# Performance work log

Measured on AMD Instinct MI355X. Metric: run time of the kernel, lower is better.

The kernel has to match this reference:

```python
import jax, jax.numpy as jnp
import numpy as np

M_MARGIN = 0.25
GAMMA = 256.0
NEG_INF = jnp.float32(-1e30)


def setup_inputs() -> dict:
    key = jax.random.key(0)
    k1, k2 = jax.random.split(key)
    feature = jax.random.normal(k1, (8192, 128), dtype=jnp.float32)
    label = jax.random.randint(k2, (8192,), 0, 64, dtype=jnp.int64)
    return {"feature": feature, "label": label}


def reference(feature, label):
    # F.normalize: L2-normalize rows (eps=1e-12)
    norm = jnp.maximum(jnp.linalg.norm(feature, axis=1, keepdims=True), 1e-12)
    f = feature / norm
    sim = f @ f.T  # [N, N]
    N = sim.shape[0]

    same = label[:, None] == label[None, :]
    triu = jnp.triu(jnp.ones((N, N), dtype=bool), k=1)
    pos_mask = same & triu
    neg_mask = (~same) & triu

    sim_d = jax.lax.stop_gradient(sim)  # .detach() in original
    ap = jnp.maximum(-sim_d + 1.0 + M_MARGIN, 0.0)
    an = jnp.maximum(sim_d + M_MARGIN, 0.0)
    delta_p = 1.0 - M_MARGIN
    delta_n = M_MARGIN

    logit_p = -ap * (sim - delta_p) * GAMMA
    logit_n = an * (sim - delta_n) * GAMMA

    # boolean-gather + logsumexp == masked logsumexp (fixed shapes, jit-friendly)
    lse_p = jax.nn.logsumexp(jnp.where(pos_mask, logit_p, NEG_INF))
    lse_n = jax.nn.logsumexp(jnp.where(neg_mask, logit_n, NEG_INF))

    return jax.nn.softplus(lse_n + lse_p)
```

## Files before the change

kernel.cpp:

```cpp
#include <hip/hip_runtime.h>
#include <hip/hip_bf16.h>
#include <math.h>

#define NROW 8192
#define DIM  128
#define BM   64
#define BN   128
#define NBLK   2080
#define NTILES (NBLK * 2)
#define NT4    (NTILES * 4)
#define NRED   32
#define PERRED (NT4 / NRED)

typedef __bf16 bf16x8 __attribute__((ext_vector_type(8)));
typedef float  f32x4  __attribute__((ext_vector_type(4)));

#define G2     369.3299304675746f
#define QPOS   (0.9375f * G2)
#define QNEG   (-0.0625f * G2)
#define NEGBIG (-3.0e38f)
#define MSENT  (-4000.0f)
#define CSTR   32

__global__ __launch_bounds__(256)
void hist_kernel(const int* __restrict__ lab, int* __restrict__ cursor) {
    __shared__ int h[4][64];
    const int tid  = threadIdx.x;
    const int w    = tid >> 6;
    const int lane = tid & 63;
    h[w][lane] = 0;
    __syncthreads();
    for (int i = tid; i < NROW; i += 256)
        atomicAdd(&h[w][lab[i]], 1);
    __syncthreads();
    if (tid < 64) {
        int tot = h[0][tid] + h[1][tid] + h[2][tid] + h[3][tid];
        int v = tot;
        #pragma unroll
        for (int off = 1; off < 64; off <<= 1) {
            int u = __shfl_up(v, off, 64);
            if (tid >= off) v += u;
        }
        cursor[tid * CSTR] = v - tot;
    }
}

__global__ __launch_bounds__(256)
void prep_kernel(const float* __restrict__ f, const int* __restrict__ lab,
                 int* __restrict__ cursor,
                 __hip_bfloat16* __restrict__ fhi, int* __restrict__ labS) {
    int row  = blockIdx.x * 4 + (threadIdx.x >> 6);
    int lane = threadIdx.x & 63;
    float2 v = ((const float2*)(f + (size_t)row * DIM))[lane];
    float ss = v.x * v.x + v.y * v.y;
    #pragma unroll
    for (int off = 32; off; off >>= 1) ss += __shfl_xor(ss, off, 64);
    float inv = 1.0f / fmaxf(sqrtf(ss), 1e-12f);
    int l = lab[row];
    int dest = 0;
    if (lane == 0) dest = atomicAdd(&cursor[l * CSTR], 1);
    dest = __shfl(dest, 0, 64);
    __hip_bfloat162 hv;
    hv.x = __float2bfloat16(v.x * inv);
    hv.y = __float2bfloat16(v.y * inv);
    ((__hip_bfloat162*)(fhi + (size_t)dest * DIM))[lane] = hv;
    if (lane == 0) labS[dest] = l;
}

__global__ __launch_bounds__(256, 2)
void sim_kernel(const __hip_bfloat16* __restrict__ fhi,
                const int* __restrict__ labS,
                float4* __restrict__ blockRes) {
    const int tid  = threadIdx.x;
    const int w    = tid >> 6;
    const int lane = tid & 63;
    const int lrow = lane & 15;
    const int lk   = lane >> 4;

    int bid = blockIdx.x;
    int tc = (int)((sqrtf(8.f * (float)bid + 1.f) - 1.f) * 0.5f);
    if (tc > 63) tc = 63;
    while (tc > 0 && bid < (tc * (tc + 1)) / 2) --tc;
    while (bid >= ((tc + 1) * (tc + 2)) / 2) ++tc;
    const int chunk = bid - (tc * (tc + 1)) / 2;
    const bool edge = (chunk == tc);

    const int colBase  = tc * BN;
    const int rowBase0 = (2 * chunk) * BM;
    const int rowBase1 = rowBase0 + BM;

    __shared__ __align__(16) char smem[64 * 1024];
    char* Bs = smem;
    char* A0 = smem + 32 * 1024;
    char* A1 = smem + 48 * 1024;

    const int rsub4 = lane >> 4;
    const int col16 = (lane & 15) << 4;

    #pragma unroll
    for (int t = 0; t < 8; ++t) {
        int seg  = w * 8 + t;
        int brow = seg * 4 + rsub4;
        const char* g = (const char*)fhi + (size_t)(colBase + brow) * 256
                      + (col16 ^ ((brow & 7) << 4));
        __builtin_amdgcn_global_load_lds(
            (const __attribute__((address_space(1))) void*)g,
            (__attribute__((address_space(3))) void*)(Bs + seg * 1024), 16, 0, 0);
    }
    #pragma unroll
    for (int t = 0; t < 4; ++t) {
        int seg  = w * 4 + t;
        int arow = seg * 4 + rsub4;
        int swz  = (col16 ^ ((arow & 7) << 4));
        const char* g0 = (const char*)fhi + (size_t)(rowBase0 + arow) * 256 + swz;
        const char* g1 = (const char*)fhi + (size_t)(rowBase1 + arow) * 256 + swz;
        __builtin_amdgcn_global_load_lds(
            (const __attribute__((address_space(1))) void*)g0,
            (__attribute__((address_space(3))) void*)(A0 + seg * 1024), 16, 0, 0);
        __builtin_amdgcn_global_load_lds(
            (const __attribute__((address_space(1))) void*)g1,
            (__attribute__((address_space(3))) void*)(A1 + seg * 1024), 16, 0, 0);
    }

    const int labCol0 = labS[colBase];
    const int labRE0  = labS[rowBase0 + BM - 1];
    const int labRE1  = labS[rowBase1 + BM - 1];

    const int ncol0 = w * 32;

    __syncthreads();

    f32x4 acc[4][2];

    #pragma unroll
    for (int ti = 0; ti < 2; ++ti) {
        const char* As      = ti ? A1 : A0;
        const int   rowBase = ti ? rowBase1 : rowBase0;
        const int   labRE   = ti ? labRE1 : labRE0;

        #pragma unroll
        for (int mi = 0; mi < 4; ++mi)
            #pragma unroll
            for (int ni = 0; ni < 2; ++ni) acc[mi][ni] = (f32x4){0.f, 0.f, 0.f, 0.f};

        #pragma unroll
        for (int q = 0; q < 4; ++q) {
            const int kb = q * 64 + lk * 16;
            bf16x8 bfr[2];
            #pragma unroll
            for (int ni = 0; ni < 2; ++ni) {
                int rb = ncol0 + ni * 16 + lrow;
                bfr[ni] = *(const bf16x8*)(Bs + rb * 256 + (kb ^ ((rb & 7) << 4)));
            }
            #pragma unroll
            for (int mi = 0; mi < 4; ++mi) {
                int ra = mi * 16 + lrow;
                bf16x8 afr = *(const bf16x8*)(As + ra * 256 + (kb ^ ((ra & 7) << 4)));
                #pragma unroll
                for (int ni = 0; ni < 2; ++ni)
                    acc[mi][ni] = __builtin_amdgcn_mfma_f32_16x16x32_bf16(
                        afr, bfr[ni], acc[mi][ni], 0, 0, 0);
            }
        }

        const bool mixed = edge || (labRE == labCol0);
        float4 res;
        if (!mixed) {
            float mx = 0.0f;
            #pragma unroll
            for (int mi = 0; mi < 4; ++mi)
                #pragma unroll
                for (int ni = 0; ni < 2; ++ni)
                    #pragma unroll
                    for (int r = 0; r < 4; ++r) {
                        float t = fmaxf(acc[mi][ni][r], -0.25f);
                        acc[mi][ni][r] = t;
                        mx = fmaxf(mx, fabsf(t));
                    }
            #pragma unroll
            for (int off = 32; off; off >>= 1)
                mx = fmaxf(mx, __shfl_xor(mx, off, 64));
            const float zc = -G2 * mx * mx;
            float sn = 0.f;
            #pragma unroll
            for (int mi = 0; mi < 4; ++mi)
                #pragma unroll
                for (int ni = 0; ni < 2; ++ni)
                    #pragma unroll
                    for (int r = 0; r < 4; ++r) {
                        float t = acc[mi][ni][r];
                        sn += __builtin_amdgcn_exp2f(fmaf(G2, t * t, zc));
                    }
            #pragma unroll
            for (int off = 32; off; off >>= 1)
                sn += __shfl_xor(sn, off, 64);
            res = make_float4(MSENT, 0.f, fmaf(G2, mx * mx, QNEG), sn);
        } else {
            int lbv[2];
            #pragma unroll
            for (int ni = 0; ni < 2; ++ni)
                lbv[ni] = labS[colBase + ncol0 + ni * 16 + lrow];
            int4 laR[4];
            #pragma unroll
            for (int mi = 0; mi < 4; ++mi)
                laR[mi] = *(const int4*)&labS[rowBase + mi * 16 + lk * 4];

            float minp = 1e30f;
            float mabs = -1.0f;

#define PASS_AB(EDGEF)                                                         \
    _Pragma("unroll")                                                          \
    for (int mi = 0; mi < 4; ++mi) {                                           \
        const int la[4] = {laR[mi].x, laR[mi].y, laR[mi].z, laR[mi].w};        \
        _Pragma("unroll")                                                      \
        for (int ni = 0; ni < 2; ++ni) {                                       \
            _Pragma("unroll")                                                  \
            for (int r = 0; r < 4; ++r) {                                      \
                float s = acc[mi][ni][r];                                      \
                bool pos = (la[r] == lbv[ni]);                                 \
                float t = fmaxf(s, -0.25f);                                    \
                bool valid = true;                                             \
                if (EDGEF) {                                                   \
                    int ig = rowBase + mi * 16 + lk * 4 + r;                   \
                    int jg = colBase + ncol0 + ni * 16 + lrow;                 \
                    valid = (jg > ig);                                         \
                    pos = pos && valid;                                        \
                }                                                              \
                float u = pos ? s : t;                                         \
                minp = fminf(minp, pos ? s : 1e30f);                           \
                bool nm = EDGEF ? (valid && !pos) : !pos;                      \
                mabs = fmaxf(mabs, nm ? fabsf(t) : -1.0f);                     \
                acc[mi][ni][r] = u;                                            \
            }                                                                  \
        }                                                                      \
    }
            if (edge) { PASS_AB(true) } else { PASS_AB(false) }
#undef PASS_AB

            #pragma unroll
            for (int off = 32; off; off >>= 1) {
                minp = fminf(minp, __shfl_xor(minp, off, 64));
                mabs = fmaxf(mabs, __shfl_xor(mabs, off, 64));
            }
            const float Mp = (minp < 2.0f)
                ? fmaf(G2, minp * minp, fmaf(-2.0f * G2, minp, QPOS)) : MSENT;
            const float Mn = (mabs >= 0.0f) ? fmaf(G2, mabs * mabs, QNEG) : MSENT;
            const float qph = QPOS - Mp;
            const float qnh = QNEG - Mn;
            float sp = 0.f, sn = 0.f;

#define PASS_B(EDGEF)                                                          \
    _Pragma("unroll")                                                          \
    for (int mi = 0; mi < 4; ++mi) {                                           \
        const int la[4] = {laR[mi].x, laR[mi].y, laR[mi].z, laR[mi].w};        \
        _Pragma("unroll")                                                      \
        for (int ni = 0; ni < 2; ++ni) {                                       \
            _Pragma("unroll")                                                  \
            for (int r = 0; r < 4; ++r) {                                      \
                float u = acc[mi][ni][r];                                      \
                bool pos = (la[r] == lbv[ni]);                                 \
                float P  = pos ? (-2.0f * G2) : 0.0f;                          \
                float Qh = pos ? qph : qnh;                                    \
                float e = __builtin_amdgcn_exp2f(                              \
                              fmaf(G2, u * u, fmaf(P, u, Qh)));                \
                if (EDGEF) {                                                   \
                    int ig = rowBase + mi * 16 + lk * 4 + r;                   \
                    int jg = colBase + ncol0 + ni * 16 + lrow;                 \
                    e = (jg > ig) ? e : 0.f;                                   \
                }                                                              \
                float ep = pos ? e : 0.f;                                      \
                sp += ep;                                                      \
                sn += (e - ep);                                                \
            }                                                                  \
        }                                                                      \
    }
            if (edge) { PASS_B(true) } else { PASS_B(false) }
#undef PASS_B

            #pragma unroll
            for (int off = 32; off; off >>= 1) {
                sp += __shfl_xor(sp, off, 64);
                sn += __shfl_xor(sn, off, 64);
            }
            res = make_float4(Mp, sp, Mn, sn);
        }
        if (lane == 0) blockRes[(bid * 2 + ti) * 4 + w] = res;
    }
}

__device__ __forceinline__ void merge2(float& m, float& s, float mo, float so) {
    float M = fmaxf(m, mo);
    s = s * __builtin_amdgcn_exp2f(m - M) + so * __builtin_amdgcn_exp2f(mo - M);
    m = M;
}

__global__ __launch_bounds__(256)
void reduce_kernel(const float4* __restrict__ in, float4* __restrict__ partial) {
    __shared__ float red[4][4];
    const int tid  = threadIdx.x;
    const int base = blockIdx.x * PERRED;
    float mp = NEGBIG, sp = 0.f, mn = NEGBIG, sn = 0.f;
    for (int i = tid; i < PERRED; i += 256) {
        float4 v = in[base + i];
        merge2(mp, sp, v.x, v.y);
        merge2(mn, sn, v.z, v.w);
    }
    #pragma unroll
    for (int off = 32; off; off >>= 1) {
        float mo = __shfl_xor(mp, off, 64), so = __shfl_xor(sp, off, 64);
        merge2(mp, sp, mo, so);
        float mo2 = __shfl_xor(mn, off, 64), so2 = __shfl_xor(sn, off, 64);
        merge2(mn, sn, mo2, so2);
    }
    const int wv = tid >> 6;
    if ((tid & 63) == 0) {
        red[wv][0] = mp; red[wv][1] = sp; red[wv][2] = mn; red[wv][3] = sn;
    }
    __syncthreads();
    if (tid == 0) {
        mp = red[0][0]; sp = red[0][1]; mn = red[0][2]; sn = red[0][3];
        #pragma unroll
        for (int q = 1; q < 4; ++q) {
            merge2(mp, sp, red[q][0], red[q][1]);
            merge2(mn, sn, red[q][2], red[q][3]);
        }
        partial[blockIdx.x] = make_float4(mp, sp, mn, sn);
    }
}

__global__ __launch_bounds__(64)
void finalize_kernel(const float4* __restrict__ partial, float* __restrict__ out) {
    const int lane = threadIdx.x;
    float mp = NEGBIG, sp = 0.f, mn = NEGBIG, sn = 0.f;
    if (lane < NRED) {
        float4 v = partial[lane];
        mp = v.x; sp = v.y; mn = v.z; sn = v.w;
    }
    #pragma unroll
    for (int off = 32; off; off >>= 1) {
        float mo = __shfl_xor(mp, off, 64), so = __shfl_xor(sp, off, 64);
        merge2(mp, sp, mo, so);
        float mo2 = __shfl_xor(mn, off, 64), so2 = __shfl_xor(sn, off, 64);
        merge2(mn, sn, mo2, so2);
    }
    if (lane == 0) {
        const double LN2 = 0.6931471805599453;
        double lse_p = ((double)mp + log2((double)sp)) * LN2;
        double lse_n = ((double)mn + log2((double)sn)) * LN2;
        double xx = lse_p + lse_n;
        double r = (xx > 30.0) ? xx : log1p(exp(xx));
        out[0] = (float)r;
    }
}

extern "C" void kernel_launch(void* const* d_in, const int* in_sizes, int n_in,
                              void* d_out, int out_size, void* d_ws, size_t ws_size,
                              hipStream_t stream) {
    const float* f   = (const float*)d_in[0];
    const int*   lab = (const int*)d_in[1];
    float*  out      = (float*)d_out;

    __hip_bfloat16* fhi = (__hip_bfloat16*)d_ws;
    int* labS    = (int*)((char*)d_ws + 2u * 1024 * 1024);
    int* cursor  = (int*)((char*)d_ws + 3u * 1024 * 1024);
    float4* blockRes = (float4*)((char*)d_ws + 4u * 1024 * 1024);
    float4* partial  = (float4*)((char*)d_ws + 8u * 1024 * 1024);

    hist_kernel<<<1, 256, 0, stream>>>(lab, cursor);
    prep_kernel<<<NROW / 4, 256, 0, stream>>>(f, lab, cursor, fhi, labS);
    sim_kernel<<<NBLK, 256, 0, stream>>>(fhi, labS, blockRes);
    reduce_kernel<<<NRED, 256, 0, stream>>>(blockRes, partial);
    finalize_kernel<<<1, 64, 0, stream>>>(partial, out);
}
```

Measured before the change: 46.74 us.

## Drop label sorting and use square 128x128 tiles with 512-thread blocks

Removes the histogram/counting-sort pass that grouped rows by label, so prep only normalizes rows in place. The similarity kernel now processes square 128x128 upper-triangular tiles with 8 waves per block and caches labels in LDS. The specialized pure-negative fast path that relied on sorted labels is gone, so every tile runs the two-pass masked logsumexp. This saves a kernel launch and atomics but adds more exp work per tile.

```diff
diff --git a/kernel.cpp b/kernel.cpp
--- a/kernel.cpp
+++ b/kernel.cpp
@@ -4,11 +4,10 @@
 
 #define NROW 8192
 #define DIM  128
-#define BM   64
-#define BN   128
-#define NBLK   2080
-#define NTILES (NBLK * 2)
-#define NT4    (NTILES * 4)
+#define BT   128
+#define NT   (NROW / BT)
+#define NBLK ((NT * (NT + 1)) / 2)
+#define NT4  (NBLK * 8)
 #define NRED   32
 #define PERRED (NT4 / NRED)
 
@@ -20,35 +19,9 @@
 #define QNEG   (-0.0625f * G2)
 #define NEGBIG (-3.0e38f)
 #define MSENT  (-4000.0f)
-#define CSTR   32
 
 __global__ __launch_bounds__(256)
-void hist_kernel(const int* __restrict__ lab, int* __restrict__ cursor) {
-    __shared__ int h[4][64];
-    const int tid  = threadIdx.x;
-    const int w    = tid >> 6;
-    const int lane = tid & 63;
-    h[w][lane] = 0;
-    __syncthreads();
-    for (int i = tid; i < NROW; i += 256)
-        atomicAdd(&h[w][lab[i]], 1);
-    __syncthreads();
-    if (tid < 64) {
-        int tot = h[0][tid] + h[1][tid] + h[2][tid] + h[3][tid];
-        int v = tot;
-        #pragma unroll
-        for (int off = 1; off < 64; off <<= 1) {
-            int u = __shfl_up(v, off, 64);
-            if (tid >= off) v += u;
-        }
-        cursor[tid * CSTR] = v - tot;
-    }
-}
-
-__global__ __launch_bounds__(256)
-void prep_kernel(const float* __restrict__ f, const int* __restrict__ lab,
-                 int* __restrict__ cursor,
-                 __hip_bfloat16* __restrict__ fhi, int* __restrict__ labS) {
+void prep_kernel(const float* __restrict__ f, __hip_bfloat16* __restrict__ fhi) {
     int row  = blockIdx.x * 4 + (threadIdx.x >> 6);
     int lane = threadIdx.x & 63;
     float2 v = ((const float2*)(f + (size_t)row * DIM))[lane];
@@ -56,20 +29,15 @@
     #pragma unroll
     for (int off = 32; off; off >>= 1) ss += __shfl_xor(ss, off, 64);
     float inv = 1.0f / fmaxf(sqrtf(ss), 1e-12f);
-    int l = lab[row];
-    int dest = 0;
-    if (lane == 0) dest = atomicAdd(&cursor[l * CSTR], 1);
-    dest = __shfl(dest, 0, 64);
     __hip_bfloat162 hv;
     hv.x = __float2bfloat16(v.x * inv);
     hv.y = __float2bfloat16(v.y * inv);
-    ((__hip_bfloat162*)(fhi + (size_t)dest * DIM))[lane] = hv;
-    if (lane == 0) labS[dest] = l;
-}
-
-__global__ __launch_bounds__(256, 2)
+    ((__hip_bfloat162*)(fhi + (size_t)row * DIM))[lane] = hv;
+}
+
+__global__ __launch_bounds__(512, 4)
 void sim_kernel(const __hip_bfloat16* __restrict__ fhi,
-                const int* __restrict__ labS,
+                const int* __restrict__ lab,
                 float4* __restrict__ blockRes) {
     const int tid  = threadIdx.x;
     const int w    = tid >> 6;
@@ -78,137 +46,85 @@
     const int lk   = lane >> 4;
 
     int bid = blockIdx.x;
-    int tc = (int)((sqrtf(8.f * (float)bid + 1.f) - 1.f) * 0.5f);
-    if (tc > 63) tc = 63;
-    while (tc > 0 && bid < (tc * (tc + 1)) / 2) --tc;
-    while (bid >= ((tc + 1) * (tc + 2)) / 2) ++tc;
-    const int chunk = bid - (tc * (tc + 1)) / 2;
-    const bool edge = (chunk == tc);
-
-    const int colBase  = tc * BN;
-    const int rowBase0 = (2 * chunk) * BM;
-    const int rowBase1 = rowBase0 + BM;
+    int tr = (int)((129.0f - sqrtf(16641.0f - 8.0f * (float)bid)) * 0.5f);
+    while (tr > 0 && bid < tr * NT - (tr * (tr - 1)) / 2) --tr;
+    while (bid >= (tr + 1) * NT - ((tr + 1) * tr) / 2) ++tr;
+    const int tc = tr + (bid - (tr * NT - (tr * (tr - 1)) / 2));
+
+    const int rowBase = tr * BT;
+    const int colBase = tc * BT;
+    const bool edge = (tr == tc);
 
     __shared__ __align__(16) char smem[64 * 1024];
-    char* Bs = smem;
-    char* A0 = smem + 32 * 1024;
-    char* A1 = smem + 48 * 1024;
+    __shared__ int labA[BT];
+    __shared__ int labB[BT];
+    char* As = smem;
+    char* Bs = smem + 32 * 1024;
+
+    if (tid < BT)            labA[tid] = lab[rowBase + tid];
+    else if (tid < 2 * BT)   labB[tid - BT] = lab[colBase + (tid - BT)];
 
     const int rsub4 = lane >> 4;
     const int col16 = (lane & 15) << 4;
 
     #pragma unroll
     for (int t = 0; t < 8; ++t) {
-        int seg  = w * 8 + t;
-        int brow = seg * 4 + rsub4;
-        const char* g = (const char*)fhi + (size_t)(colBase + brow) * 256
-                      + (col16 ^ ((brow & 7) << 4));
+        int seg = w * 8 + t;
+        int arr = seg >> 5;
+        int s32 = seg & 31;
+        int row = s32 * 4 + rsub4;
+        const char* g = (const char*)fhi
+            + (size_t)((arr ? colBase : rowBase) + row) * 256
+            + (col16 ^ ((row & 7) << 4));
+        char* ldsb = (arr ? Bs : As) + s32 * 1024;
         __builtin_amdgcn_global_load_lds(
             (const __attribute__((address_space(1))) void*)g,
-            (__attribute__((address_space(3))) void*)(Bs + seg * 1024), 16, 0, 0);
-    }
-    #pragma unroll
-    for (int t = 0; t < 4; ++t) {
-        int seg  = w * 4 + t;
-        int arow = seg * 4 + rsub4;
-        int swz  = (col16 ^ ((arow & 7) << 4));
-        const char* g0 = (const char*)fhi + (size_t)(rowBase0 + arow) * 256 + swz;
-        const char* g1 = (const char*)fhi + (size_t)(rowBase1 + arow) * 256 + swz;
-        __builtin_amdgcn_global_load_lds(
-            (const __attribute__((address_space(1))) void*)g0,
-            (__attribute__((address_space(3))) void*)(A0 + seg * 1024), 16, 0, 0);
-        __builtin_amdgcn_global_load_lds(
-            (const __attribute__((address_space(1))) void*)g1,
-            (__attribute__((address_space(3))) void*)(A1 + seg * 1024), 16, 0, 0);
-    }
-
-    const int labCol0 = labS[colBase];
-    const int labRE0  = labS[rowBase0 + BM - 1];
-    const int labRE1  = labS[rowBase1 + BM - 1];
-
-    const int ncol0 = w * 32;
+            (__attribute__((address_space(3))) void*)ldsb, 16, 0, 0);
+    }
+
+    f32x4 acc[4][2];
+    #pragma unroll
+    for (int mi = 0; mi < 4; ++mi)
+        #pragma unroll
+        for (int ni = 0; ni < 2; ++ni) acc[mi][ni] = (f32x4){0.f, 0.f, 0.f, 0.f};
+
+    const int mrow0 = (w >> 2) * 64;
+    const int ncol0 = (w & 3) * 32;
 
     __syncthreads();
 
-    f32x4 acc[4][2];
-
-    #pragma unroll
-    for (int ti = 0; ti < 2; ++ti) {
-        const char* As      = ti ? A1 : A0;
-        const int   rowBase = ti ? rowBase1 : rowBase0;
-        const int   labRE   = ti ? labRE1 : labRE0;
-
-        #pragma unroll
-        for (int mi = 0; mi < 4; ++mi)
-            #pragma unroll
-            for (int ni = 0; ni < 2; ++ni) acc[mi][ni] = (f32x4){0.f, 0.f, 0.f, 0.f};
-
-        #pragma unroll
-        for (int q = 0; q < 4; ++q) {
-            const int kb = q * 64 + lk * 16;
-            bf16x8 bfr[2];
-            #pragma unroll
-            for (int ni = 0; ni < 2; ++ni) {
-                int rb = ncol0 + ni * 16 + lrow;
-                bfr[ni] = *(const bf16x8*)(Bs + rb * 256 + (kb ^ ((rb & 7) << 4)));
-            }
-            #pragma unroll
-            for (int mi = 0; mi < 4; ++mi) {
-                int ra = mi * 16 + lrow;
-                bf16x8 afr = *(const bf16x8*)(As + ra * 256 + (kb ^ ((ra & 7) << 4)));
-                #pragma unroll
-                for (int ni = 0; ni < 2; ++ni)
-                    acc[mi][ni] = __builtin_amdgcn_mfma_f32_16x16x32_bf16(
-                        afr, bfr[ni], acc[mi][ni], 0, 0, 0);
-            }
+    #pragma unroll
+    for (int q = 0; q < 4; ++q) {
+        const int kb = q * 64 + lk * 16;
+        bf16x8 bfr[2];
+        #pragma unroll
+        for (int ni = 0; ni < 2; ++ni) {
+            int rb = ncol0 + ni * 16 + lrow;
+            bfr[ni] = *(const bf16x8*)(Bs + rb * 256 + (kb ^ ((rb & 7) << 4)));
         }
-
-        const bool mixed = edge || (labRE == labCol0);
-        float4 res;
-        if (!mixed) {
-            float mx = 0.0f;
-            #pragma unroll
-            for (int mi = 0; mi < 4; ++mi)
-                #pragma unroll
-                for (int ni = 0; ni < 2; ++ni)
-                    #pragma unroll
-                    for (int r = 0; r < 4; ++r) {
-                        float t = fmaxf(acc[mi][ni][r], -0.25f);
-                        acc[mi][ni][r] = t;
-                        mx = fmaxf(mx, fabsf(t));
-                    }
-            #pragma unroll
-            for (int off = 32; off; off >>= 1)
-                mx = fmaxf(mx, __shfl_xor(mx, off, 64));
-            const float zc = -G2 * mx * mx;
-            float sn = 0.f;
-            #pragma unroll
-            for (int mi = 0; mi < 4; ++mi)
-                #pragma unroll
-                for (int ni = 0; ni < 2; ++ni)
-                    #pragma unroll
-                    for (int r = 0; r < 4; ++r) {
-                        float t = acc[mi][ni][r];
-                        sn += __builtin_amdgcn_exp2f(fmaf(G2, t * t, zc));
-                    }
-            #pragma unroll
-            for (int off = 32; off; off >>= 1)
-                sn += __shfl_xor(sn, off, 64);
-            res = make_float4(MSENT, 0.f, fmaf(G2, mx * mx, QNEG), sn);
-        } else {
-            int lbv[2];
+        #pragma unroll
+        for (int mi = 0; mi < 4; ++mi) {
+            int ra = mrow0 + mi * 16 + lrow;
+            bf16x8 afr = *(const bf16x8*)(As + ra * 256 + (kb ^ ((ra & 7) << 4)));
             #pragma unroll
             for (int ni = 0; ni < 2; ++ni)
-                lbv[ni] = labS[colBase + ncol0 + ni * 16 + lrow];
-            int4 laR[4];
-            #pragma unroll
-            for (int mi = 0; mi < 4; ++mi)
-                laR[mi] = *(const int4*)&labS[rowBase + mi * 16 + lk * 4];
-
-            float minp = 1e30f;
-            float mabs = -1.0f;
-
-#define PASS_AB(EDGEF)                                                         \
+                acc[mi][ni] = __builtin_amdgcn_mfma_f32_16x16x32_bf16(
+                    afr, bfr[ni], acc[mi][ni], 0, 0, 0);
+        }
+    }
+
+    int lbv[2];
+    #pragma unroll
+    for (int ni = 0; ni < 2; ++ni) lbv[ni] = labB[ncol0 + ni * 16 + lrow];
+    int4 laR[4];
+    #pragma unroll
+    for (int mi = 0; mi < 4; ++mi)
+        laR[mi] = *(const int4*)&labA[mrow0 + mi * 16 + lk * 4];
+
+    float minp = 1e30f;
+    float mabs = -1.0f;
+
+#define PASS_A(EDGEF)                                                          \
     _Pragma("unroll")                                                          \
     for (int mi = 0; mi < 4; ++mi) {                                           \
         const int la[4] = {laR[mi].x, laR[mi].y, laR[mi].z, laR[mi].w};        \
@@ -221,9 +137,9 @@
                 float t = fmaxf(s, -0.25f);                                    \
                 bool valid = true;                                             \
                 if (EDGEF) {                                                   \
-                    int ig = rowBase + mi * 16 + lk * 4 + r;                   \
-                    int jg = colBase + ncol0 + ni * 16 + lrow;                 \
-                    valid = (jg > ig);                                         \
+                    int il = mrow0 + mi * 16 + lk * 4 + r;                     \
+                    int jl = ncol0 + ni * 16 + lrow;                           \
+                    valid = (jl > il);                                         \
                     pos = pos && valid;                                        \
                 }                                                              \
                 float u = pos ? s : t;                                         \
@@ -234,20 +150,20 @@
             }                                                                  \
         }                                                                      \
     }
-            if (edge) { PASS_AB(true) } else { PASS_AB(false) }
-#undef PASS_AB
-
-            #pragma unroll
-            for (int off = 32; off; off >>= 1) {
-                minp = fminf(minp, __shfl_xor(minp, off, 64));
-                mabs = fmaxf(mabs, __shfl_xor(mabs, off, 64));
-            }
-            const float Mp = (minp < 2.0f)
-                ? fmaf(G2, minp * minp, fmaf(-2.0f * G2, minp, QPOS)) : MSENT;
-            const float Mn = (mabs >= 0.0f) ? fmaf(G2, mabs * mabs, QNEG) : MSENT;
-            const float qph = QPOS - Mp;
-            const float qnh = QNEG - Mn;
-            float sp = 0.f, sn = 0.f;
+    if (edge) { PASS_A(true) } else { PASS_A(false) }
+#undef PASS_A
+
+    #pragma unroll
+    for (int off = 32; off; off >>= 1) {
+        minp = fminf(minp, __shfl_xor(minp, off, 64));
+        mabs = fmaxf(mabs, __shfl_xor(mabs, off, 64));
+    }
+    const float Mp = (minp < 2.0f)
+        ? fmaf(G2, minp * minp, fmaf(-2.0f * G2, minp, QPOS)) : MSENT;
+    const float Mn = (mabs >= 0.0f) ? fmaf(G2, mabs * mabs, QNEG) : MSENT;
+    const float qph = QPOS - Mp;
+    const float qnh = QNEG - Mn;
+    float sp = 0.f, sn = 0.f;
 
 #define PASS_B(EDGEF)                                                          \
     _Pragma("unroll")                                                          \
@@ -264,9 +180,9 @@
                 float e = __builtin_amdgcn_exp2f(                              \
                               fmaf(G2, u * u, fmaf(P, u, Qh)));                \
                 if (EDGEF) {                                                   \
-                    int ig = rowBase + mi * 16 + lk * 4 + r;                   \
-                    int jg = colBase + ncol0 + ni * 16 + lrow;                 \
-                    e = (jg > ig) ? e : 0.f;                                   \
+                    int il = mrow0 + mi * 16 + lk * 4 + r;                     \
+                    int jl = ncol0 + ni * 16 + lrow;                           \
+                    e = (jl > il) ? e : 0.f;                                   \
                 }                                                              \
                 float ep = pos ? e : 0.f;                                      \
                 sp += ep;                                                      \
@@ -274,18 +190,15 @@
             }                                                                  \
         }                                                                      \
     }
-            if (edge) { PASS_B(true) } else { PASS_B(false) }
+    if (edge) { PASS_B(true) } else { PASS_B(false) }
 #undef PASS_B
 
-            #pragma unroll
-            for (int off = 32; off; off >>= 1) {
-                sp += __shfl_xor(sp, off, 64);
-                sn += __shfl_xor(sn, off, 64);
-            }
-            res = make_float4(Mp, sp, Mn, sn);
-        }
-        if (lane == 0) blockRes[(bid * 2 + ti) * 4 + w] = res;
-    }
+    #pragma unroll
+    for (int off = 32; off; off >>= 1) {
+        sp += __shfl_xor(sp, off, 64);
+        sn += __shfl_xor(sn, off, 64);
+    }
+    if (lane == 0) blockRes[bid * 8 + w] = make_float4(Mp, sp, Mn, sn);
 }
 
 __device__ __forceinline__ void merge2(float& m, float& s, float mo, float so) {
@@ -361,14 +274,11 @@
     float*  out      = (float*)d_out;
 
     __hip_bfloat16* fhi = (__hip_bfloat16*)d_ws;
-    int* labS    = (int*)((char*)d_ws + 2u * 1024 * 1024);
-    int* cursor  = (int*)((char*)d_ws + 3u * 1024 * 1024);
     float4* blockRes = (float4*)((char*)d_ws + 4u * 1024 * 1024);
     float4* partial  = (float4*)((char*)d_ws + 8u * 1024 * 1024);
 
-    hist_kernel<<<1, 256, 0, stream>>>(lab, cursor);
-    prep_kernel<<<NROW / 4, 256, 0, stream>>>(f, lab, cursor, fhi, labS);
-    sim_kernel<<<NBLK, 256, 0, stream>>>(fhi, labS, blockRes);
+    prep_kernel<<<NROW / 4, 256, 0, stream>>>(f, fhi);
+    sim_kernel<<<NBLK, 512, 0, stream>>>(fhi, lab, blockRes);
     reduce_kernel<<<NRED, 256, 0, stream>>>(blockRes, partial);
     finalize_kernel<<<1, 64, 0, stream>>>(partial, out);
 }
```

Measured after the change: 45.43 us. 2.8% less time.
